# Optimization experiments

Measured on AMD Instinct MI355X. Metric: run time of the kernel, lower is better.

Reference implementation:

```python
import jax, jax.numpy as jnp
import numpy as np

N = 100000
E = 1600000
F = 64
THETA = (0.6, -0.4, 0.3, -0.2, 0.1)  # k = 5 polynomial coefficients


def setup_inputs() -> dict:
    key = jax.random.key(0)
    kx, ke = jax.random.split(key)
    x = jax.random.normal(kx, (N, F), dtype=jnp.float32)
    edge_index = jax.random.randint(ke, (2, E), 0, N, dtype=jnp.int64)
    return {"x": x, "edge_index": edge_index}


def _l_sym_mul(feat, src, dst, deg_inv_sqrt, n):
    # L_sym * feat = feat - D^{-1/2} A D^{-1/2} feat
    src_norm = feat[src] * deg_inv_sqrt[src]            # [E, F] gather + scale
    agg = jax.ops.segment_sum(src_norm, dst, num_segments=n)  # scatter-add to dst
    return feat - deg_inv_sqrt * agg


def reference(x, edge_index):
    src, dst = edge_index[0], edge_index[1]
    n = x.shape[0]
    # in-degree from dst, clamp to >= 1, D^{-1/2} as [N, 1]
    deg = jax.ops.segment_sum(jnp.ones((src.shape[0],), dtype=x.dtype), dst,
                              num_segments=n)
    deg = jnp.maximum(deg, 1.0)[:, None]
    deg_inv_sqrt = deg ** -0.5

    h_acc = THETA[0] * x
    feat = x
    for k in range(1, len(THETA)):
        feat = _l_sym_mul(feat, src, dst, deg_inv_sqrt, n)
        h_acc = h_acc + THETA[k] * feat
    return h_acc
```

## Files before the change

kernel.cpp:

```cpp
#include <hip/hip_runtime.h>


constexpr int kF = 64;
constexpr int BSHIFT = 9;
constexpr int BW = 1 << BSHIFT;
constexpr int TILE = 4096;

static __device__ __forceinline__ float bfl(unsigned u) {
    return __uint_as_float(u << 16);
}
static __device__ __forceinline__ float bfh(unsigned u) {
    return __uint_as_float(u & 0xffff0000u);
}
static __device__ __forceinline__ unsigned f2bf(float f) {
    unsigned u = __float_as_uint(f);
    return (u + 0x7fffu + ((u >> 16) & 1u)) >> 16;
}
static __device__ __forceinline__ unsigned pack2(float a, float b) {
    return f2bf(a) | (f2bf(b) << 16);
}

__global__ void k_zero_i(int* __restrict__ p, int n) {
    int i = blockIdx.x * blockDim.x + threadIdx.x;
    if (i < n) p[i] = 0;
}

__global__ void k_cvt(const float4* __restrict__ x4, uint4* __restrict__ xb4, int n8) {
    int i = blockIdx.x * blockDim.x + threadIdx.x;
    if (i < n8) {
        float4 a = x4[2 * i];
        float4 b = x4[2 * i + 1];
        uint4 o;
        o.x = pack2(a.x, a.y);
        o.y = pack2(a.z, a.w);
        o.z = pack2(b.x, b.y);
        o.w = pack2(b.z, b.w);
        xb4[i] = o;
    }
}

__global__ void k_binA(const int* __restrict__ src, const int* __restrict__ dst,
                       unsigned* __restrict__ pairs, int* __restrict__ gcursor,
                       int E, int K, int cap) {
    __shared__ unsigned sorted[TILE];
    __shared__ int hist[256];
    __shared__ int stmp[256];
    __shared__ int loff[257];
    __shared__ int lcur[256];
    __shared__ int gb[256];
    const int tid = threadIdx.x;
    const long long tb = (long long)blockIdx.x * TILE;
    const int tcount = (int)min((long long)TILE, (long long)E - tb);

    if (tid < 256) hist[tid] = 0;
    __syncthreads();
    for (int i = tid; i < tcount; i += 512)
        atomicAdd(&hist[dst[tb + i] >> BSHIFT], 1);
    __syncthreads();
    int v = (tid < 256) ? hist[tid] : 0;
    if (tid < 256) stmp[tid] = v;
    __syncthreads();
    for (int o = 1; o < 256; o <<= 1) {
        int t = (tid >= o && tid < 256) ? stmp[tid - o] : 0;
        __syncthreads();
        if (tid < 256) stmp[tid] += t;
        __syncthreads();
    }
    if (tid < 256) {
        loff[tid] = stmp[tid] - v;
        lcur[tid] = stmp[tid] - v;
        gb[tid] = (tid < K) ? atomicAdd(&gcursor[tid], v) : 0;
        if (tid == 255) loff[256] = stmp[255];
    }
    __syncthreads();
    for (int i = tid; i < tcount; i += 512) {
        int d = dst[tb + i];
        int s = src[tb + i];
        int b = d >> BSHIFT;
        int pos = atomicAdd(&lcur[b], 1);
        sorted[pos] = ((unsigned)(d & (BW - 1)) << 23) | (unsigned)s;
    }
    __syncthreads();
    for (int i = tid; i < tcount; i += 512) {
        int lo = 0, hi = K - 1;
        while (lo < hi) {
            int mid = (lo + hi + 1) >> 1;
            if (loff[mid] <= i) lo = mid; else hi = mid - 1;
        }
        pairs[(size_t)lo * cap + gb[lo] + (i - loff[lo])] = sorted[i];
    }
}

__global__ void k_binB(const unsigned* __restrict__ pairs, const int* __restrict__ gcursor,
                       int* __restrict__ rp, float* __restrict__ dinv,
                       int* __restrict__ csr, int N, int E, int K, int cap) {
    __shared__ int gsc[256];
    __shared__ int cnt[BW];
    __shared__ int stmp[BW];
    __shared__ int excl[BW];
    __shared__ int cur[BW];
    const int b = blockIdx.x;
    const int tid = threadIdx.x;

    int gv = (tid < 256) ? ((tid < K) ? gcursor[tid] : 0) : 0;
    if (tid < 256) gsc[tid] = gv;
    __syncthreads();
    for (int o = 1; o < 256; o <<= 1) {
        int t = (tid >= o && tid < 256) ? gsc[tid - o] : 0;
        __syncthreads();
        if (tid < 256) gsc[tid] += t;
        __syncthreads();
    }
    const int ecnt = gcursor[b];
    const int base = gsc[b] - ecnt;
    const unsigned* bp = pairs + (size_t)b * cap;

    cnt[tid] = 0;
    __syncthreads();
    for (int i = tid; i < ecnt; i += BW)
        atomicAdd(&cnt[bp[i] >> 23], 1);
    __syncthreads();
    int v = cnt[tid];
    stmp[tid] = v;
    __syncthreads();
    for (int o = 1; o < BW; o <<= 1) {
        int t = (tid >= o) ? stmp[tid - o] : 0;
        __syncthreads();
        stmp[tid] += t;
        __syncthreads();
    }
    excl[tid] = stmp[tid] - v;
    cur[tid] = stmp[tid] - v;
    __syncthreads();
    for (int i = tid; i < ecnt; i += BW) {
        unsigned p = bp[i];
        int pos = atomicAdd(&cur[p >> 23], 1);
        csr[base + pos] = (int)(p & 0x7FFFFFu);
    }
    int node = (b << BSHIFT) + tid;
    if (node < N) {
        rp[node] = base + excl[tid];
        dinv[node] = rsqrtf(fmaxf((float)v, 1.0f));
    }
    if (b == K - 1 && tid == 0) rp[N] = E;
}

template <bool FIRST, bool LAST>
__global__ void k_gather(const int* __restrict__ rp, const int* __restrict__ csr,
                         const unsigned short* __restrict__ featin,
                         const float* __restrict__ xf,
                         const float* __restrict__ dinv,
                         unsigned short* __restrict__ featout,
                         float* __restrict__ h,
                         int n, float th0, float theta) {
    int wid = (blockIdx.x * blockDim.x + threadIdx.x) >> 6;
    int lane = threadIdx.x & 63;
    int half = lane >> 5;
    int r = (lane >> 3) & 3;
    int c = lane & 7;
    int node = wid * 2 + half;
    if (wid * 2 >= n) return;
    bool valid = node < n;
    int beg = valid ? rp[node] : 0;
    int end = valid ? rp[node + 1] : 0;
    int len = end - beg;
    int olen = __shfl_xor(len, 32, 64);
    int mlen = (len > olen) ? len : olen;

    float acc[8] = {0.f, 0.f, 0.f, 0.f, 0.f, 0.f, 0.f, 0.f};
    for (int i = 0; i < mlen; i += 4) {
        int j = beg + i + r;
        bool ok = j < end;
        int jj = ok ? j : 0;
        int s = csr[jj];
        float w = ok ? dinv[s] : 0.0f;
        uint4 rr = *(const uint4*)(featin + ((size_t)s << 6) + (c << 3));
        acc[0] += w * bfl(rr.x);
        acc[1] += w * bfh(rr.x);
        acc[2] += w * bfl(rr.y);
        acc[3] += w * bfh(rr.y);
        acc[4] += w * bfl(rr.z);
        acc[5] += w * bfh(rr.z);
        acc[6] += w * bfl(rr.w);
        acc[7] += w * bfh(rr.w);
    }
    #pragma unroll
    for (int m = 8; m <= 16; m <<= 1) {
        #pragma unroll
        for (int i = 0; i < 8; ++i)
            acc[i] += __shfl_xor(acc[i], m, 64);
    }

    if (r == 0 && valid) {
        size_t off = ((size_t)node << 6) + (c << 3);
        float f[8];
        if (FIRST) {
            float4 a = *(const float4*)(xf + off);
            float4 b = *(const float4*)(xf + off + 4);
            f[0] = a.x; f[1] = a.y; f[2] = a.z; f[3] = a.w;
            f[4] = b.x; f[5] = b.y; f[6] = b.z; f[7] = b.w;
        } else {
            uint4 rr = *(const uint4*)(featin + off);
            f[0] = bfl(rr.x); f[1] = bfh(rr.x);
            f[2] = bfl(rr.y); f[3] = bfh(rr.y);
            f[4] = bfl(rr.z); f[5] = bfh(rr.z);
            f[6] = bfl(rr.w); f[7] = bfh(rr.w);
        }
        float di = dinv[node];
        float v[8];
        #pragma unroll
        for (int i = 0; i < 8; ++i) v[i] = f[i] - di * acc[i];
        float4 h0, h1;
        if (FIRST) {
            h0 = make_float4(th0 * f[0] + theta * v[0], th0 * f[1] + theta * v[1],
                             th0 * f[2] + theta * v[2], th0 * f[3] + theta * v[3]);
            h1 = make_float4(th0 * f[4] + theta * v[4], th0 * f[5] + theta * v[5],
                             th0 * f[6] + theta * v[6], th0 * f[7] + theta * v[7]);
        } else {
            h0 = *(const float4*)(h + off);
            h1 = *(const float4*)(h + off + 4);
            h0.x += theta * v[0]; h0.y += theta * v[1];
            h0.z += theta * v[2]; h0.w += theta * v[3];
            h1.x += theta * v[4]; h1.y += theta * v[5];
            h1.z += theta * v[6]; h1.w += theta * v[7];
        }
        *(float4*)(h + off) = h0;
        *(float4*)(h + off + 4) = h1;
        if (!LAST) {
            uint4 o;
            o.x = pack2(v[0], v[1]);
            o.y = pack2(v[2], v[3]);
            o.z = pack2(v[4], v[5]);
            o.w = pack2(v[6], v[7]);
            *(uint4*)(featout + off) = o;
        }
    }
}

extern "C" void kernel_launch(void* const* d_in, const int* in_sizes, int n_in,
                              void* d_out, int out_size, void* d_ws, size_t ws_size,
                              hipStream_t stream) {
    const float* x  = (const float*)d_in[0];
    const int*   ei = (const int*)d_in[1];
    const int N = in_sizes[0] / kF;
    const int E = in_sizes[1] / 2;
    const int* src = ei;
    const int* dst = ei + E;
    float* h = (float*)d_out;

    const int K = (N + BW - 1) >> BSHIFT;
    const int cap = 2 * ((E + K - 1) / K);

    char* ws = (char*)d_ws;
    size_t off = 0;
    auto carve = [&](size_t bytes) {
        void* p = ws + off;
        off = (off + bytes + 511) & ~(size_t)511;
        return p;
    };
    int*            gcursor = (int*)carve((size_t)K * 4);
    int*            rp      = (int*)carve((size_t)(N + 1) * 4);
    float*          dinv    = (float*)carve((size_t)N * 4);
    int*            csr     = (int*)carve((size_t)E * 4);
    unsigned short* xb      = (unsigned short*)carve((size_t)N * kF * 2);
    unsigned short* featA   = (unsigned short*)carve((size_t)N * kF * 2);
    unsigned short* featB   = (unsigned short*)carve((size_t)N * kF * 2);
    unsigned*       pairs   = (unsigned*)carve((size_t)K * cap * 4);

    const float theta[5] = {0.6f, -0.4f, 0.3f, -0.2f, 0.1f};

    k_zero_i<<<1, 256, 0, stream>>>(gcursor, K);
    k_binA<<<(E + TILE - 1) / TILE, 512, 0, stream>>>(src, dst, pairs, gcursor, E, K, cap);
    k_binB<<<K, BW, 0, stream>>>(pairs, gcursor, rp, dinv, csr, N, E, K, cap);
    const int n8 = N * kF / 8;
    k_cvt<<<(n8 + 255) / 256, 256, 0, stream>>>((const float4*)x, (uint4*)xb, n8);

    const int nwaves = (N + 1) / 2;
    const int gblocks = (nwaves + 3) / 4;
    k_gather<true, false><<<gblocks, 256, 0, stream>>>(rp, csr, xb, x, dinv, featA, h,
                                                       N, theta[0], theta[1]);
    k_gather<false, false><<<gblocks, 256, 0, stream>>>(rp, csr, featA, nullptr, dinv, featB, h,
                                                        N, 0.f, theta[2]);
    k_gather<false, false><<<gblocks, 256, 0, stream>>>(rp, csr, featB, nullptr, dinv, featA, h,
                                                        N, 0.f, theta[3]);
    k_gather<false, true><<<gblocks, 256, 0, stream>>>(rp, csr, featA, nullptr, dinv, nullptr, h,
                                                       N, 0.f, theta[4]);
}
```

Baseline: 293.2 us.

## Fuse bf16 conversion into binning, shrink buckets to 256 nodes, unroll gather by two

The separate fp32-to-bf16 conversion kernel is folded into k_binA, with each block converting a slice of x, which removes one launch. The dst bucket width drops from 512 to 256 nodes. That doubles the bucket count to about 391, gives k_binB more, smaller blocks, and widens the k_binA histogram and scan to 512 entries. The gather loop now processes two neighbours per lane per iteration so more independent loads are in flight, at the cost of more wasted work on short rows.

```diff
diff --git a/kernel.cpp b/kernel.cpp
--- a/kernel.cpp
+++ b/kernel.cpp
@@ -2,9 +2,10 @@
 
 
 constexpr int kF = 64;
-constexpr int BSHIFT = 9;
-constexpr int BW = 1 << BSHIFT;
+constexpr int BSHIFT = 8;
+constexpr int NB = 1 << BSHIFT;
 constexpr int TILE = 4096;
+constexpr int KMAX = 512;
 
 static __device__ __forceinline__ float bfl(unsigned u) {
     return __uint_as_float(u << 16);
@@ -25,60 +26,61 @@
     if (i < n) p[i] = 0;
 }
 
-__global__ void k_cvt(const float4* __restrict__ x4, uint4* __restrict__ xb4, int n8) {
-    int i = blockIdx.x * blockDim.x + threadIdx.x;
-    if (i < n8) {
-        float4 a = x4[2 * i];
-        float4 b = x4[2 * i + 1];
-        uint4 o;
-        o.x = pack2(a.x, a.y);
-        o.y = pack2(a.z, a.w);
-        o.z = pack2(b.x, b.y);
-        o.w = pack2(b.z, b.w);
-        xb4[i] = o;
-    }
-}
-
 __global__ void k_binA(const int* __restrict__ src, const int* __restrict__ dst,
                        unsigned* __restrict__ pairs, int* __restrict__ gcursor,
-                       int E, int K, int cap) {
+                       const float4* __restrict__ x4, uint4* __restrict__ xb4,
+                       int n8, int E, int K, int cap) {
     __shared__ unsigned sorted[TILE];
-    __shared__ int hist[256];
-    __shared__ int stmp[256];
-    __shared__ int loff[257];
-    __shared__ int lcur[256];
-    __shared__ int gb[256];
+    __shared__ int hist[KMAX];
+    __shared__ int stmp[KMAX];
+    __shared__ int loff[KMAX + 1];
+    __shared__ int lcur[KMAX];
+    __shared__ int gb[KMAX];
     const int tid = threadIdx.x;
     const long long tb = (long long)blockIdx.x * TILE;
     const int tcount = (int)min((long long)TILE, (long long)E - tb);
 
-    if (tid < 256) hist[tid] = 0;
+    {
+        int per = (n8 + gridDim.x - 1) / (int)gridDim.x;
+        int b0 = blockIdx.x * per;
+        int b1 = min(b0 + per, n8);
+        for (int i = b0 + tid; i < b1; i += 512) {
+            float4 a = x4[2 * i];
+            float4 b = x4[2 * i + 1];
+            uint4 o;
+            o.x = pack2(a.x, a.y);
+            o.y = pack2(a.z, a.w);
+            o.z = pack2(b.x, b.y);
+            o.w = pack2(b.z, b.w);
+            xb4[i] = o;
+        }
+    }
+
+    hist[tid] = 0;
     __syncthreads();
     for (int i = tid; i < tcount; i += 512)
         atomicAdd(&hist[dst[tb + i] >> BSHIFT], 1);
     __syncthreads();
-    int v = (tid < 256) ? hist[tid] : 0;
-    if (tid < 256) stmp[tid] = v;
-    __syncthreads();
-    for (int o = 1; o < 256; o <<= 1) {
-        int t = (tid >= o && tid < 256) ? stmp[tid - o] : 0;
-        __syncthreads();
-        if (tid < 256) stmp[tid] += t;
-        __syncthreads();
-    }
-    if (tid < 256) {
-        loff[tid] = stmp[tid] - v;
-        lcur[tid] = stmp[tid] - v;
-        gb[tid] = (tid < K) ? atomicAdd(&gcursor[tid], v) : 0;
-        if (tid == 255) loff[256] = stmp[255];
-    }
+    int v = hist[tid];
+    stmp[tid] = v;
+    __syncthreads();
+    for (int o = 1; o < KMAX; o <<= 1) {
+        int t = (tid >= o) ? stmp[tid - o] : 0;
+        __syncthreads();
+        stmp[tid] += t;
+        __syncthreads();
+    }
+    loff[tid] = stmp[tid] - v;
+    lcur[tid] = stmp[tid] - v;
+    gb[tid] = (tid < K) ? atomicAdd(&gcursor[tid], v) : 0;
+    if (tid == KMAX - 1) loff[KMAX] = stmp[KMAX - 1];
     __syncthreads();
     for (int i = tid; i < tcount; i += 512) {
         int d = dst[tb + i];
         int s = src[tb + i];
         int b = d >> BSHIFT;
         int pos = atomicAdd(&lcur[b], 1);
-        sorted[pos] = ((unsigned)(d & (BW - 1)) << 23) | (unsigned)s;
+        sorted[pos] = ((unsigned)(d & (NB - 1)) << 23) | (unsigned)s;
     }
     __syncthreads();
     for (int i = tid; i < tcount; i += 512) {
@@ -94,51 +96,53 @@
 __global__ void k_binB(const unsigned* __restrict__ pairs, const int* __restrict__ gcursor,
                        int* __restrict__ rp, float* __restrict__ dinv,
                        int* __restrict__ csr, int N, int E, int K, int cap) {
-    __shared__ int gsc[256];
-    __shared__ int cnt[BW];
-    __shared__ int stmp[BW];
-    __shared__ int excl[BW];
-    __shared__ int cur[BW];
+    __shared__ int gsc[KMAX];
+    __shared__ int cnt[NB];
+    __shared__ int stmp[NB];
+    __shared__ int excl[NB];
+    __shared__ int cur[NB];
     const int b = blockIdx.x;
     const int tid = threadIdx.x;
 
-    int gv = (tid < 256) ? ((tid < K) ? gcursor[tid] : 0) : 0;
-    if (tid < 256) gsc[tid] = gv;
-    __syncthreads();
-    for (int o = 1; o < 256; o <<= 1) {
-        int t = (tid >= o && tid < 256) ? gsc[tid - o] : 0;
-        __syncthreads();
-        if (tid < 256) gsc[tid] += t;
+    int gv = (tid < K) ? gcursor[tid] : 0;
+    gsc[tid] = gv;
+    __syncthreads();
+    for (int o = 1; o < KMAX; o <<= 1) {
+        int t = (tid >= o) ? gsc[tid - o] : 0;
+        __syncthreads();
+        gsc[tid] += t;
         __syncthreads();
     }
     const int ecnt = gcursor[b];
     const int base = gsc[b] - ecnt;
     const unsigned* bp = pairs + (size_t)b * cap;
 
-    cnt[tid] = 0;
-    __syncthreads();
-    for (int i = tid; i < ecnt; i += BW)
+    if (tid < NB) cnt[tid] = 0;
+    __syncthreads();
+    for (int i = tid; i < ecnt; i += 512)
         atomicAdd(&cnt[bp[i] >> 23], 1);
     __syncthreads();
-    int v = cnt[tid];
-    stmp[tid] = v;
-    __syncthreads();
-    for (int o = 1; o < BW; o <<= 1) {
-        int t = (tid >= o) ? stmp[tid - o] : 0;
-        __syncthreads();
-        stmp[tid] += t;
-        __syncthreads();
-    }
-    excl[tid] = stmp[tid] - v;
-    cur[tid] = stmp[tid] - v;
-    __syncthreads();
-    for (int i = tid; i < ecnt; i += BW) {
+    int v = (tid < NB) ? cnt[tid] : 0;
+    if (tid < NB) stmp[tid] = v;
+    __syncthreads();
+    for (int o = 1; o < NB; o <<= 1) {
+        int t = (tid >= o && tid < NB) ? stmp[tid - o] : 0;
+        __syncthreads();
+        if (tid < NB) stmp[tid] += t;
+        __syncthreads();
+    }
+    if (tid < NB) {
+        excl[tid] = stmp[tid] - v;
+        cur[tid] = stmp[tid] - v;
+    }
+    __syncthreads();
+    for (int i = tid; i < ecnt; i += 512) {
         unsigned p = bp[i];
         int pos = atomicAdd(&cur[p >> 23], 1);
         csr[base + pos] = (int)(p & 0x7FFFFFu);
     }
     int node = (b << BSHIFT) + tid;
-    if (node < N) {
+    if (tid < NB && node < N) {
         rp[node] = base + excl[tid];
         dinv[node] = rsqrtf(fmaxf((float)v, 1.0f));
     }
@@ -168,21 +172,33 @@
     int mlen = (len > olen) ? len : olen;
 
     float acc[8] = {0.f, 0.f, 0.f, 0.f, 0.f, 0.f, 0.f, 0.f};
-    for (int i = 0; i < mlen; i += 4) {
-        int j = beg + i + r;
-        bool ok = j < end;
-        int jj = ok ? j : 0;
-        int s = csr[jj];
-        float w = ok ? dinv[s] : 0.0f;
-        uint4 rr = *(const uint4*)(featin + ((size_t)s << 6) + (c << 3));
-        acc[0] += w * bfl(rr.x);
-        acc[1] += w * bfh(rr.x);
-        acc[2] += w * bfl(rr.y);
-        acc[3] += w * bfh(rr.y);
-        acc[4] += w * bfl(rr.z);
-        acc[5] += w * bfh(rr.z);
-        acc[6] += w * bfl(rr.w);
-        acc[7] += w * bfh(rr.w);
+    for (int i = 0; i < mlen; i += 8) {
+        int j1 = beg + i + r;
+        int j2 = j1 + 4;
+        bool ok1 = j1 < end;
+        bool ok2 = j2 < end;
+        int s1 = csr[ok1 ? j1 : 0];
+        int s2 = csr[ok2 ? j2 : 0];
+        float w1 = ok1 ? dinv[s1] : 0.0f;
+        float w2 = ok2 ? dinv[s2] : 0.0f;
+        uint4 ra = *(const uint4*)(featin + ((size_t)s1 << 6) + (c << 3));
+        uint4 rb = *(const uint4*)(featin + ((size_t)s2 << 6) + (c << 3));
+        acc[0] += w1 * bfl(ra.x);
+        acc[1] += w1 * bfh(ra.x);
+        acc[2] += w1 * bfl(ra.y);
+        acc[3] += w1 * bfh(ra.y);
+        acc[4] += w1 * bfl(ra.z);
+        acc[5] += w1 * bfh(ra.z);
+        acc[6] += w1 * bfl(ra.w);
+        acc[7] += w1 * bfh(ra.w);
+        acc[0] += w2 * bfl(rb.x);
+        acc[1] += w2 * bfh(rb.x);
+        acc[2] += w2 * bfl(rb.y);
+        acc[3] += w2 * bfh(rb.y);
+        acc[4] += w2 * bfl(rb.z);
+        acc[5] += w2 * bfh(rb.z);
+        acc[6] += w2 * bfl(rb.w);
+        acc[7] += w2 * bfh(rb.w);
     }
     #pragma unroll
     for (int m = 8; m <= 16; m <<= 1) {
@@ -248,7 +264,7 @@
     const int* dst = ei + E;
     float* h = (float*)d_out;
 
-    const int K = (N + BW - 1) >> BSHIFT;
+    const int K = (N + NB - 1) >> BSHIFT;
     const int cap = 2 * ((E + K - 1) / K);
 
     char* ws = (char*)d_ws;
@@ -269,11 +285,12 @@
 
     const float theta[5] = {0.6f, -0.4f, 0.3f, -0.2f, 0.1f};
 
-    k_zero_i<<<1, 256, 0, stream>>>(gcursor, K);
-    k_binA<<<(E + TILE - 1) / TILE, 512, 0, stream>>>(src, dst, pairs, gcursor, E, K, cap);
-    k_binB<<<K, BW, 0, stream>>>(pairs, gcursor, rp, dinv, csr, N, E, K, cap);
     const int n8 = N * kF / 8;
-    k_cvt<<<(n8 + 255) / 256, 256, 0, stream>>>((const float4*)x, (uint4*)xb, n8);
+    k_zero_i<<<1, 512, 0, stream>>>(gcursor, K);
+    k_binA<<<(E + TILE - 1) / TILE, 512, 0, stream>>>(src, dst, pairs, gcursor,
+                                                      (const float4*)x, (uint4*)xb,
+                                                      n8, E, K, cap);
+    k_binB<<<K, 512, 0, stream>>>(pairs, gcursor, rp, dinv, csr, N, E, K, cap);
 
     const int nwaves = (N + 1) / 2;
     const int gblocks = (nwaves + 3) / 4;
```

Measured after the change: 273.9 us. 1.07x faster.
